# Kernel tuning notes

Hardware: AMD Instinct MI355X
Metric: run time of the kernel (lower is better)

The kernel has to match this reference:

```python
import jax, jax.numpy as jnp
import numpy as np

L, B, N, IN, H, ATTN, RED, OUT = 3, 8, 512, 64, 128, 32, 32, 3


def setup_inputs() -> dict:
    key = jax.random.key(0)
    ks = jax.random.split(key, 34)
    def rn(i, shape, s=0.05):
        return jax.random.normal(ks[i], shape, dtype=jnp.float32) * s
    inp = {
        "X": rn(0, (B, N, IN), 1.0),
        # sparse binary adjacency (avg degree ~10) and denser clique graph
        "A": (jax.random.uniform(ks[1], (B, N, N)) < 0.02).astype(jnp.float32),
        "Ac": (jax.random.uniform(ks[2], (B, N, N)) < 0.05).astype(jnp.float32),
        # topo embedding
        "embed_w": rn(3, (H, IN)), "embed_b": jnp.zeros((H,), jnp.float32),
        "topo_eps": jnp.zeros((1,), jnp.float32),
        "topo_w": rn(4, (H, H)), "topo_b": jnp.zeros((H,), jnp.float32),
        "theta": rn(5, (H, 2)),
        # per-layer dual GIN (index 0: A, index 1: Ac)
        "gin_eps": jnp.zeros((L, 2, 1), jnp.float32),
        "gin_w": rn(6, (L, 2, H, H)), "gin_b": jnp.zeros((L, 2, H), jnp.float32),
        # per-layer flexible attention
        "wo": rn(7, (L, ATTN, H)), "w1": rn(8, (L, ATTN, H)),
        "wphi": rn(9, (L, ATTN)),
        "wy_w": rn(10, (L, H, H)), "wy_b": jnp.zeros((L, H), jnp.float32),
        "we_w": rn(11, (L, H, ATTN)), "we_b": jnp.zeros((L, H), jnp.float32),
        # per-layer SE block
        "lin1_w": rn(12, (L, RED, H)), "lin1_b": jnp.zeros((L, RED), jnp.float32),
        "lin2_w": rn(13, (L, H, RED)), "lin2_b": jnp.zeros((L, H), jnp.float32),
        "mlp_w": rn(14, (L, H, H)), "mlp_b": jnp.zeros((L, H), jnp.float32),
        # node head
        "head1_w": rn(15, (H // 2, H)), "head1_b": jnp.zeros((H // 2,), jnp.float32),
        "head2_w": rn(16, (OUT, H // 2)), "head2_b": jnp.zeros((OUT,), jnp.float32),
    }
    return inp


def _lin(x, w, b=None):
    y = x @ w.T
    return y if b is None else y + b


def _gin(x, a, eps, w, b):
    # (1+eps)*X + A@X, then Linear, then ReLU
    return jax.nn.relu(_lin((1.0 + eps) * x + a @ x, w, b))


def _forward(X, A, Ac, embed_w, embed_b, topo_eps, topo_w, topo_b, theta,
             gin_eps, gin_w, gin_b, wo, w1, wphi, wy_w, wy_b, we_w, we_b,
             lin1_w, lin1_b, lin2_w, lin2_b, mlp_w, mlp_b,
             head1_w, head1_b, head2_w, head2_b):
    # TopoPositionalEmbedding (shared GIN on both graphs)
    Xh = _lin(X, embed_w, embed_b)                      # (B,N,H)
    hA = _gin(Xh, A, topo_eps[0], topo_w, topo_b)
    hAC = _gin(Xh, Ac, topo_eps[0], topo_w, topo_b)
    Xp = Xh + jnp.tanh(hA * theta[:, 0]) + jnp.tanh(hAC * theta[:, 1])

    for l in range(L):
        # dual GIN
        XA = _gin(Xp, A, gin_eps[l, 0, 0], gin_w[l, 0], gin_b[l, 0])
        XAC = _gin(Xp, Ac, gin_eps[l, 1, 0], gin_w[l, 1], gin_b[l, 1])
        # GRIT-style flexible attention
        ho = Xp @ wo[l].T                               # (B,N,ATTN)
        h1 = Xp @ w1[l].T
        e = jnp.tanh(ho[:, :, None, :] + h1[:, None, :, :])   # (B,N,N,ATTN)
        alpha = jax.nn.softmax(e @ wphi[l], axis=-1)    # (B,N,N)
        Xy = _lin(Xp, wy_w[l], wy_b[l])                 # (B,N,H)
        # sum_j alpha_ij * We(e_ij) == We(sum_j alpha_ij * e_ij) since We is affine
        # and sum_j alpha_ij == 1 (avoids the (B,N,N,H) intermediate)
        ctx = jnp.einsum('bij,bijd->bid', alpha, e)     # (B,N,ATTN)
        Xatt = alpha @ Xy + _lin(ctx, we_w[l], we_b[l])
        Xbar = XA + XAC + Xatt
        # SE gating
        y1 = jax.nn.relu(_lin(Xbar.sum(axis=1), lin1_w[l], lin1_b[l]))
        y2 = jax.nn.sigmoid(_lin(y1, lin2_w[l], lin2_b[l]))
        Xp = _lin(Xbar * y2[:, None, :], mlp_w[l], mlp_b[l])

    h = jax.nn.relu(_lin(Xp, head1_w, head1_b))
    return _lin(h, head2_w, head2_b)                    # (B,N,OUT)


def reference(X, A, Ac, embed_w, embed_b, topo_eps, topo_w, topo_b, theta,
              gin_eps, gin_w, gin_b, wo, w1, wphi, wy_w, wy_b, we_w, we_b,
              lin1_w, lin1_b, lin2_w, lin2_b, mlp_w, mlp_b,
              head1_w, head1_b, head2_w, head2_b):
    return _forward(X, A, Ac, embed_w, embed_b, topo_eps, topo_w, topo_b, theta,
                    gin_eps, gin_w, gin_b, wo, w1, wphi, wy_w, wy_b, we_w, we_b,
                    lin1_w, lin1_b, lin2_w, lin2_b, mlp_w, mlp_b,
                    head1_w, head1_b, head2_w, head2_b)
```

## Files before the change

kernel.cpp:

```cpp
#include <hip/hip_runtime.h>

#define Bc 8
#define Nc 512
#define INc 64
#define Hc 128
#define Atc 32
#define REDc 32
#define OUTc 3
#define Lc 3
#define MNc (Bc * Nc)

__device__ __forceinline__ float tanh_fast(float x) {
    float e = __expf(2.f * x);
    return 1.f - 2.f * __builtin_amdgcn_rcpf(e + 1.f);
}

template <int TM, int K, int ACT>
__global__ __launch_bounds__(256) void gemm256(
        const float* __restrict__ X, const float* __restrict__ W,
        const float* __restrict__ bias, float* __restrict__ Y,
        const float* __restrict__ scale) {
    constexpr int RPG = TM / 2;
    __shared__ float xs[TM * K];
    int m0 = blockIdx.x * TM;
    int t = threadIdx.x;
    const float* sc = scale ? scale + (size_t)(m0 >> 9) * K : nullptr;
    for (int idx4 = t; idx4 < TM * K / 4; idx4 += 256) {
        float4 v = ((const float4*)(X + (size_t)m0 * K))[idx4];
        if (sc) {
            int base = idx4 * 4;
            v.x *= sc[base & (K - 1)]; v.y *= sc[(base + 1) & (K - 1)];
            v.z *= sc[(base + 2) & (K - 1)]; v.w *= sc[(base + 3) & (K - 1)];
        }
        ((float4*)xs)[idx4] = v;
    }
    __syncthreads();
    int n = t & 127;
    int grp = t >> 7;
    float bv = bias ? bias[n] : 0.f;
    float acc[RPG];
#pragma unroll
    for (int r = 0; r < RPG; ++r) acc[r] = bv;
    const float* w = W + (size_t)n * K;
    for (int k = 0; k < K; k += 4) {
        float4 wv = *(const float4*)(w + k);
#pragma unroll
        for (int r = 0; r < RPG; ++r) {
            float4 xv = *(const float4*)(xs + (grp * RPG + r) * K + k);
            acc[r] = fmaf(xv.x, wv.x, acc[r]); acc[r] = fmaf(xv.y, wv.y, acc[r]);
            acc[r] = fmaf(xv.z, wv.z, acc[r]); acc[r] = fmaf(xv.w, wv.w, acc[r]);
        }
    }
#pragma unroll
    for (int r = 0; r < RPG; ++r) {
        float v = acc[r];
        if (ACT) v = fmaxf(v, 0.f);
        Y[(size_t)(m0 + grp * RPG + r) * 128 + n] = v;
    }
}

__global__ __launch_bounds__(128) void spmm2(
        const float* __restrict__ A, const float* __restrict__ Acg,
        const float* __restrict__ X, const float* __restrict__ eA,
        const float* __restrict__ eC, float* __restrict__ T1, float* __restrict__ T2) {
    int bi = blockIdx.x;
    int b = bi >> 9;
    int h = threadIdx.x;
    __shared__ int idxA[Nc], idxC[Nc];
    __shared__ int cntA, cntC;
    if (h == 0) { cntA = 0; cntC = 0; }
    __syncthreads();
    {
        float4 a4 = ((const float4*)(A + (size_t)bi * Nc))[h];
        if (a4.x != 0.f) idxA[atomicAdd(&cntA, 1)] = 4 * h;
        if (a4.y != 0.f) idxA[atomicAdd(&cntA, 1)] = 4 * h + 1;
        if (a4.z != 0.f) idxA[atomicAdd(&cntA, 1)] = 4 * h + 2;
        if (a4.w != 0.f) idxA[atomicAdd(&cntA, 1)] = 4 * h + 3;
        float4 c4 = ((const float4*)(Acg + (size_t)bi * Nc))[h];
        if (c4.x != 0.f) idxC[atomicAdd(&cntC, 1)] = 4 * h;
        if (c4.y != 0.f) idxC[atomicAdd(&cntC, 1)] = 4 * h + 1;
        if (c4.z != 0.f) idxC[atomicAdd(&cntC, 1)] = 4 * h + 2;
        if (c4.w != 0.f) idxC[atomicAdd(&cntC, 1)] = 4 * h + 3;
    }
    __syncthreads();
    int nA = cntA, nC = cntC;
    const float* Xb = X + (size_t)b * Nc * Hc;
    float a1 = 0.f, a2 = 0.f;
    for (int q = 0; q < nA; ++q) a1 += Xb[(size_t)idxA[q] * Hc + h];
    for (int q = 0; q < nC; ++q) a2 += Xb[(size_t)idxC[q] * Hc + h];
    size_t o = (size_t)bi * Hc + h;
    float xv = X[o];
    T1[o] = (1.f + eA[0]) * xv + a1;
    T2[o] = (1.f + eC[0]) * xv + a2;
}

__global__ __launch_bounds__(256) void gemm2_topo(
        const float* __restrict__ T1, const float* __restrict__ T2,
        const float* __restrict__ W, const float* __restrict__ bias,
        const float* __restrict__ Xh, const float* __restrict__ theta,
        float* __restrict__ Xp) {
    __shared__ float xs1[8 * Hc], xs2[8 * Hc];
    int m0 = blockIdx.x * 8;
    int t = threadIdx.x;
    for (int idx4 = t; idx4 < 8 * Hc / 4; idx4 += 256) {
        ((float4*)xs1)[idx4] = ((const float4*)(T1 + (size_t)m0 * Hc))[idx4];
        ((float4*)xs2)[idx4] = ((const float4*)(T2 + (size_t)m0 * Hc))[idx4];
    }
    __syncthreads();
    int n = t & 127, grp = t >> 7;
    float bv = bias[n];
    float ac1[4], ac2[4];
#pragma unroll
    for (int r = 0; r < 4; ++r) { ac1[r] = bv; ac2[r] = bv; }
    const float* w = W + (size_t)n * Hc;
    for (int k = 0; k < Hc; k += 4) {
        float4 wv = *(const float4*)(w + k);
#pragma unroll
        for (int r = 0; r < 4; ++r) {
            float4 x1 = *(const float4*)(xs1 + (grp * 4 + r) * Hc + k);
            float4 x2 = *(const float4*)(xs2 + (grp * 4 + r) * Hc + k);
            ac1[r] = fmaf(x1.x, wv.x, ac1[r]); ac1[r] = fmaf(x1.y, wv.y, ac1[r]);
            ac1[r] = fmaf(x1.z, wv.z, ac1[r]); ac1[r] = fmaf(x1.w, wv.w, ac1[r]);
            ac2[r] = fmaf(x2.x, wv.x, ac2[r]); ac2[r] = fmaf(x2.y, wv.y, ac2[r]);
            ac2[r] = fmaf(x2.z, wv.z, ac2[r]); ac2[r] = fmaf(x2.w, wv.w, ac2[r]);
        }
    }
    float th0 = theta[2 * n], th1 = theta[2 * n + 1];
#pragma unroll
    for (int r = 0; r < 4; ++r) {
        size_t o = (size_t)(m0 + grp * 4 + r) * Hc + n;
        float g1 = fmaxf(ac1[r], 0.f), g2 = fmaxf(ac2[r], 0.f);
        Xp[o] = Xh[o] + tanh_fast(g1 * th0) + tanh_fast(g2 * th1);
    }
}

__global__ __launch_bounds__(256) void gemm2_gin(
        const float* __restrict__ T1, const float* __restrict__ T2,
        const float* __restrict__ W1, const float* __restrict__ b1,
        const float* __restrict__ W2, const float* __restrict__ b2,
        float* __restrict__ GS) {
    __shared__ float xs1[8 * Hc], xs2[8 * Hc];
    int m0 = blockIdx.x * 8;
    int t = threadIdx.x;
    for (int idx4 = t; idx4 < 8 * Hc / 4; idx4 += 256) {
        ((float4*)xs1)[idx4] = ((const float4*)(T1 + (size_t)m0 * Hc))[idx4];
        ((float4*)xs2)[idx4] = ((const float4*)(T2 + (size_t)m0 * Hc))[idx4];
    }
    __syncthreads();
    int n = t & 127, grp = t >> 7;
    float ac1[4], ac2[4];
    float bv1 = b1[n], bv2 = b2[n];
#pragma unroll
    for (int r = 0; r < 4; ++r) { ac1[r] = bv1; ac2[r] = bv2; }
    const float* w1 = W1 + (size_t)n * Hc;
    const float* w2 = W2 + (size_t)n * Hc;
    for (int k = 0; k < Hc; k += 4) {
        float4 wv1 = *(const float4*)(w1 + k);
        float4 wv2 = *(const float4*)(w2 + k);
#pragma unroll
        for (int r = 0; r < 4; ++r) {
            float4 x1 = *(const float4*)(xs1 + (grp * 4 + r) * Hc + k);
            float4 x2 = *(const float4*)(xs2 + (grp * 4 + r) * Hc + k);
            ac1[r] = fmaf(x1.x, wv1.x, ac1[r]); ac1[r] = fmaf(x1.y, wv1.y, ac1[r]);
            ac1[r] = fmaf(x1.z, wv1.z, ac1[r]); ac1[r] = fmaf(x1.w, wv1.w, ac1[r]);
            ac2[r] = fmaf(x2.x, wv2.x, ac2[r]); ac2[r] = fmaf(x2.y, wv2.y, ac2[r]);
            ac2[r] = fmaf(x2.z, wv2.z, ac2[r]); ac2[r] = fmaf(x2.w, wv2.w, ac2[r]);
        }
    }
#pragma unroll
    for (int r = 0; r < 4; ++r) {
        size_t o = (size_t)(m0 + grp * 4 + r) * Hc + n;
        GS[o] = fmaxf(ac1[r], 0.f) + fmaxf(ac2[r], 0.f);
    }
}

__global__ __launch_bounds__(256) void qkv_gemm(
        const float* __restrict__ Xp, const float* __restrict__ wy_w,
        const float* __restrict__ wy_b, const float* __restrict__ wo,
        const float* __restrict__ w1, float* __restrict__ Xy,
        float* __restrict__ hov, float* __restrict__ h1v) {
    __shared__ float xs[8 * Hc];
    int m0 = blockIdx.x * 8;
    int t = threadIdx.x;
    for (int idx4 = t; idx4 < 8 * Hc / 4; idx4 += 256)
        ((float4*)xs)[idx4] = ((const float4*)(Xp + (size_t)m0 * Hc))[idx4];
    __syncthreads();
    {
        int n = t & 127, grp = t >> 7;
        float bv = wy_b[n];
        float acc[4];
#pragma unroll
        for (int r = 0; r < 4; ++r) acc[r] = bv;
        const float* w = wy_w + (size_t)n * Hc;
        for (int k = 0; k < Hc; k += 4) {
            float4 wv = *(const float4*)(w + k);
#pragma unroll
            for (int r = 0; r < 4; ++r) {
                float4 xv = *(const float4*)(xs + (grp * 4 + r) * Hc + k);
                acc[r] = fmaf(xv.x, wv.x, acc[r]); acc[r] = fmaf(xv.y, wv.y, acc[r]);
                acc[r] = fmaf(xv.z, wv.z, acc[r]); acc[r] = fmaf(xv.w, wv.w, acc[r]);
            }
        }
#pragma unroll
        for (int r = 0; r < 4; ++r)
            Xy[(size_t)(m0 + grp * 4 + r) * Hc + n] = acc[r];
    }
    {
        int n2 = t & 63, g2 = t >> 6;
        const float* w = (n2 < 32) ? (wo + (size_t)n2 * Hc) : (w1 + (size_t)(n2 - 32) * Hc);
        float acc[2] = {0.f, 0.f};
        for (int k = 0; k < Hc; k += 4) {
            float4 wv = *(const float4*)(w + k);
#pragma unroll
            for (int r = 0; r < 2; ++r) {
                float4 xv = *(const float4*)(xs + (g2 * 2 + r) * Hc + k);
                acc[r] = fmaf(xv.x, wv.x, acc[r]); acc[r] = fmaf(xv.y, wv.y, acc[r]);
                acc[r] = fmaf(xv.z, wv.z, acc[r]); acc[r] = fmaf(xv.w, wv.w, acc[r]);
            }
        }
#pragma unroll
        for (int r = 0; r < 2; ++r) {
            int m = m0 + g2 * 2 + r;
            float v = tanh_fast(acc[r]);
            if (n2 < 32) hov[(size_t)m * Atc + n2] = v;
            else h1v[(size_t)m * Atc + (n2 - 32)] = v;
        }
    }
}

__global__ __launch_bounds__(256) void attn_part(
        const float* __restrict__ ta, const float* __restrict__ tb,
        const float* __restrict__ wphi, const float* __restrict__ Xy,
        float* __restrict__ Pp, float* __restrict__ ctxp, float* __restrict__ wsp) {
    int blk = blockIdx.x;
    int b = blk >> 7;
    int r6 = (blk >> 1) & 63;
    int js = blk & 1;
    int i0 = r6 * 8;
    int t = threadIdx.x;
    __shared__ float als[8 * 256];
    __shared__ float4 red4[1024];
    __shared__ float tas[8 * 32];
    tas[t] = ta[((size_t)b * Nc + i0) * 32 + t];
    __syncthreads();
    {
        int i = t >> 5;
        int kq = t & 3;
        int jl = (t >> 2) & 7;
        float4 wp0 = ((const float4*)wphi)[kq * 2];
        float4 wp1 = ((const float4*)wphi)[kq * 2 + 1];
        float4 ta0 = *(const float4*)(tas + i * 32 + kq * 8);
        float4 ta1 = *(const float4*)(tas + i * 32 + kq * 8 + 4);
        const float* tbb = tb + ((size_t)b * Nc + js * 256) * 32;
        const float4* p = (const float4*)(tbb + (size_t)jl * 32 + kq * 8);
        float4 ra = p[0], rb = p[1];
        float ca[8];
#pragma unroll
        for (int q = 0; q < 8; ++q) ca[q] = 0.f;
        float wsum = 0.f;
#pragma unroll 2
        for (int jj = 0; jj < 32; ++jj) {
            float4 ha = ra, hb = rb;
            p += 64;
            if (jj < 31) { ra = p[0]; rb = p[1]; }
            float e0 = (ta0.x + ha.x) * __builtin_amdgcn_rcpf(fmaf(ta0.x, ha.x, 1.f));
            float e1 = (ta0.y + ha.y) * __builtin_amdgcn_rcpf(fmaf(ta0.y, ha.y, 1.f));
            float e2 = (ta0.z + ha.z) * __builtin_amdgcn_rcpf(fmaf(ta0.z, ha.z, 1.f));
            float e3 = (ta0.w + ha.w) * __builtin_amdgcn_rcpf(fmaf(ta0.w, ha.w, 1.f));
            float e4 = (ta1.x + hb.x) * __builtin_amdgcn_rcpf(fmaf(ta1.x, hb.x, 1.f));
            float e5 = (ta1.y + hb.y) * __builtin_amdgcn_rcpf(fmaf(ta1.y, hb.y, 1.f));
            float e6 = (ta1.z + hb.z) * __builtin_amdgcn_rcpf(fmaf(ta1.z, hb.z, 1.f));
            float e7 = (ta1.w + hb.w) * __builtin_amdgcn_rcpf(fmaf(ta1.w, hb.w, 1.f));
            float sc = e0 * wp0.x;
            sc = fmaf(e1, wp0.y, sc);
            sc = fmaf(e2, wp0.z, sc);
            sc = fmaf(e3, wp0.w, sc);
            sc = fmaf(e4, wp1.x, sc);
            sc = fmaf(e5, wp1.y, sc);
            sc = fmaf(e6, wp1.z, sc);
            sc = fmaf(e7, wp1.w, sc);
            sc += __shfl_xor(sc, 1);
            sc += __shfl_xor(sc, 2);
            float w = __expf(sc);
            if (kq == 0) als[i * 256 + jj * 8 + jl] = w;
            wsum += w;
            ca[0] = fmaf(w, e0, ca[0]);
            ca[1] = fmaf(w, e1, ca[1]);
            ca[2] = fmaf(w, e2, ca[2]);
            ca[3] = fmaf(w, e3, ca[3]);
            ca[4] = fmaf(w, e4, ca[4]);
            ca[5] = fmaf(w, e5, ca[5]);
            ca[6] = fmaf(w, e6, ca[6]);
            ca[7] = fmaf(w, e7, ca[7]);
        }
#pragma unroll
        for (int o = 16; o > 0; o >>= 1) wsum += __shfl_xor(wsum, o);
        if ((t & 31) == 0) wsp[(size_t)js * MNc + (size_t)b * Nc + i0 + i] = wsum;
#pragma unroll
        for (int q = 0; q < 8; ++q) {
            ca[q] += __shfl_xor(ca[q], 4);
            ca[q] += __shfl_xor(ca[q], 8);
            ca[q] += __shfl_xor(ca[q], 16);
        }
        if (jl == 0) {
            float* cp = ctxp + ((size_t)js * MNc + (size_t)b * Nc + i0 + i) * 32 + kq * 8;
#pragma unroll
            for (int q = 0; q < 8; ++q) cp[q] = ca[q];
        }
    }
    __syncthreads();
    {
        int h4 = t & 31, jg = t >> 5;
        const float* Xyb = Xy + ((size_t)b * Nc + js * 256) * Hc;
        float* Pb = Pp + (size_t)js * MNc * Hc;
#pragma unroll 1
        for (int c = 0; c < 2; ++c) {
            float4 acc[4];
#pragma unroll
            for (int r = 0; r < 4; ++r) acc[r] = make_float4(0.f, 0.f, 0.f, 0.f);
#pragma unroll 2
            for (int jq = 0; jq < 32; ++jq) {
                int j = jg * 32 + jq;
                float4 x = *(const float4*)(Xyb + (size_t)j * Hc + h4 * 4);
#pragma unroll
                for (int r = 0; r < 4; ++r) {
                    float av = als[(c * 4 + r) * 256 + j];
                    acc[r].x = fmaf(av, x.x, acc[r].x);
                    acc[r].y = fmaf(av, x.y, acc[r].y);
                    acc[r].z = fmaf(av, x.z, acc[r].z);
                    acc[r].w = fmaf(av, x.w, acc[r].w);
                }
            }
#pragma unroll
            for (int r = 0; r < 4; ++r) red4[jg * 128 + r * 32 + h4] = acc[r];
            __syncthreads();
            if (t < 128) {
                int ii = t >> 5, hq = t & 31;
                float4 s = red4[ii * 32 + hq];
#pragma unroll
                for (int gq = 1; gq < 8; ++gq) {
                    float4 p = red4[gq * 128 + ii * 32 + hq];
                    s.x += p.x; s.y += p.y; s.z += p.z; s.w += p.w;
                }
                *(float4*)(Pb + ((size_t)b * Nc + i0 + c * 4 + ii) * Hc + hq * 4) = s;
            }
            __syncthreads();
        }
    }
}

__global__ __launch_bounds__(256) void attn_combine(
        const float* __restrict__ Pp, const float* __restrict__ ctxp,
        const float* __restrict__ wsp, const float* __restrict__ we_w,
        const float* __restrict__ we_b, const float* __restrict__ GS,
        float* __restrict__ Xbar) {
    int m0 = blockIdx.x * 8;
    int t = threadIdx.x;
    __shared__ float ctxs[8 * 32];
    __shared__ float sinv[8];
    if (t < 8) sinv[t] = 4.f / (wsp[m0 + t] + wsp[MNc + m0 + t]);
    ctxs[t] = ctxp[(size_t)m0 * 32 + t] + ctxp[(size_t)MNc * 32 + (size_t)m0 * 32 + t];
    __syncthreads();
    int ii = t >> 5, hq = t & 31;
    size_t o = (size_t)(m0 + ii) * Hc + hq * 4;
    float4 p0 = *(const float4*)(Pp + o);
    float4 p1 = *(const float4*)(Pp + (size_t)MNc * Hc + o);
    float si = sinv[ii];
    const float* c = ctxs + ii * 32;
    float wec[4];
#pragma unroll
    for (int ho_ = 0; ho_ < 4; ++ho_) {
        const float4* wrow = (const float4*)(we_w + (size_t)(hq * 4 + ho_) * 32);
        float sv = 0.f;
#pragma unroll
        for (int q = 0; q < 8; ++q) {
            float4 w4 = wrow[q];
            sv = fmaf(w4.x, c[4 * q], sv); sv = fmaf(w4.y, c[4 * q + 1], sv);
            sv = fmaf(w4.z, c[4 * q + 2], sv); sv = fmaf(w4.w, c[4 * q + 3], sv);
        }
        wec[ho_] = sv;
    }
    float4 wb = *(const float4*)(we_b + hq * 4);
    float4 gv = *(const float4*)(GS + o);
    float4 outv;
    outv.x = (p0.x + p1.x + wec[0]) * si + wb.x + gv.x;
    outv.y = (p0.y + p1.y + wec[1]) * si + wb.y + gv.y;
    outv.z = (p0.z + p1.z + wec[2]) * si + wb.z + gv.z;
    outv.w = (p0.w + p1.w + wec[3]) * si + wb.w + gv.w;
    *(float4*)(Xbar + o) = outv;
}

__global__ __launch_bounds__(256) void se_part(
        const float* __restrict__ Xbar, float* __restrict__ part) {
    int blk = blockIdx.x;
    int b = blk >> 4, p = blk & 15;
    int t = threadIdx.x;
    int h = t & 127, half = t >> 7;
    __shared__ float s2[256];
    const float* Xb = Xbar + ((size_t)b * Nc + p * 32 + half * 16) * Hc;
    float acc = 0.f;
    for (int i = 0; i < 16; ++i) acc += Xb[(size_t)i * Hc + h];
    s2[t] = acc;
    __syncthreads();
    if (t < 128) part[(size_t)blk * Hc + t] = s2[t] + s2[t + 128];
}

__global__ __launch_bounds__(128) void se_mlp(
        const float* __restrict__ part, const float* __restrict__ l1w,
        const float* __restrict__ l1b, const float* __restrict__ l2w,
        const float* __restrict__ l2b, float* __restrict__ y2) {
    int b = blockIdx.x;
    int t = threadIdx.x;
    __shared__ float s[Hc];
    __shared__ float y1s[REDc];
    const float* pb = part + (size_t)b * 16 * Hc;
    float acc = 0.f;
#pragma unroll
    for (int p = 0; p < 16; ++p) acc += pb[p * Hc + t];
    s[t] = acc;
    __syncthreads();
    if (t < REDc) {
        float a = l1b[t];
        const float* w = l1w + (size_t)t * Hc;
        for (int k = 0; k < Hc; ++k) a = fmaf(s[k], w[k], a);
        y1s[t] = fmaxf(a, 0.f);
    }
    __syncthreads();
    {
        float a = l2b[t];
        const float* w2 = l2w + (size_t)t * REDc;
#pragma unroll
        for (int k = 0; k < REDc; ++k) a = fmaf(y1s[k], w2[k], a);
        y2[(size_t)b * Hc + t] = 1.f / (1.f + __expf(-a));
    }
}

__global__ __launch_bounds__(64) void head_kernel(const float* __restrict__ Xp, const float* __restrict__ h1w,
                            const float* __restrict__ h1b, const float* __restrict__ h2w,
                            const float* __restrict__ h2b, float* __restrict__ out) {
    int m = blockIdx.x;
    int t = threadIdx.x;
    __shared__ float xs[Hc];
    __shared__ float hs[64];
    xs[t] = Xp[(size_t)m * Hc + t];
    xs[t + 64] = Xp[(size_t)m * Hc + t + 64];
    __syncthreads();
    float a = h1b[t];
    const float* w = h1w + (size_t)t * Hc;
    for (int k = 0; k < Hc; ++k) a = fmaf(xs[k], w[k], a);
    hs[t] = fmaxf(a, 0.f);
    __syncthreads();
    if (t < OUTc) {
        float o = h2b[t];
        const float* w2 = h2w + (size_t)t * 64;
#pragma unroll
        for (int k = 0; k < 64; ++k) o = fmaf(hs[k], w2[k], o);
        out[(size_t)m * OUTc + t] = o;
    }
}

extern "C" void kernel_launch(void* const* d_in, const int* in_sizes, int n_in,
                              void* d_out, int out_size, void* d_ws, size_t ws_size,
                              hipStream_t stream) {
    const float* X       = (const float*)d_in[0];
    const float* A       = (const float*)d_in[1];
    const float* Acg     = (const float*)d_in[2];
    const float* embed_w = (const float*)d_in[3];
    const float* embed_b = (const float*)d_in[4];
    const float* topo_eps= (const float*)d_in[5];
    const float* topo_w  = (const float*)d_in[6];
    const float* topo_b  = (const float*)d_in[7];
    const float* theta   = (const float*)d_in[8];
    const float* gin_eps = (const float*)d_in[9];
    const float* gin_w   = (const float*)d_in[10];
    const float* gin_b   = (const float*)d_in[11];
    const float* wo      = (const float*)d_in[12];
    const float* w1      = (const float*)d_in[13];
    const float* wphi    = (const float*)d_in[14];
    const float* wy_w    = (const float*)d_in[15];
    const float* wy_b    = (const float*)d_in[16];
    const float* we_w    = (const float*)d_in[17];
    const float* we_b    = (const float*)d_in[18];
    const float* lin1_w  = (const float*)d_in[19];
    const float* lin1_b  = (const float*)d_in[20];
    const float* lin2_w  = (const float*)d_in[21];
    const float* lin2_b  = (const float*)d_in[22];
    const float* mlp_w   = (const float*)d_in[23];
    const float* mlp_b   = (const float*)d_in[24];
    const float* head1_w = (const float*)d_in[25];
    const float* head1_b = (const float*)d_in[26];
    const float* head2_w = (const float*)d_in[27];
    const float* head2_b = (const float*)d_in[28];
    float* out = (float*)d_out;

    float* ws = (float*)d_ws;
    const int MN = Bc * Nc;
    const size_t SZ = (size_t)MN * Hc;
    float* Xh   = ws;
    float* Xp   = Xh + SZ;
    float* T1   = Xp + SZ;
    float* T2   = T1 + SZ;
    float* GS   = T2 + SZ;
    float* Xy   = GS + SZ;
    float* hov  = Xy + SZ;
    float* h1v  = hov + (size_t)MN * Atc;
    float* y2   = h1v + (size_t)MN * Atc;
    float* part = y2 + (size_t)Bc * Hc;
    float* Pp   = part + (size_t)Bc * 16 * Hc;
    float* ctxp = Pp + 2 * SZ;
    float* wsp  = ctxp + (size_t)2 * MN * Atc;
    float* Xbar = T1;

    gemm256<8, INc, 0><<<MN / 8, 256, 0, stream>>>(X, embed_w, embed_b, Xh, nullptr);
    spmm2<<<MN, 128, 0, stream>>>(A, Acg, Xh, topo_eps, topo_eps, T1, T2);
    gemm2_topo<<<MN / 8, 256, 0, stream>>>(T1, T2, topo_w, topo_b, Xh, theta, Xp);

    for (int l = 0; l < Lc; ++l) {
        spmm2<<<MN, 128, 0, stream>>>(A, Acg, Xp, gin_eps + l * 2, gin_eps + l * 2 + 1, T1, T2);
        gemm2_gin<<<MN / 8, 256, 0, stream>>>(T1, T2,
            gin_w + (size_t)(l * 2 + 0) * Hc * Hc, gin_b + (size_t)(l * 2 + 0) * Hc,
            gin_w + (size_t)(l * 2 + 1) * Hc * Hc, gin_b + (size_t)(l * 2 + 1) * Hc, GS);
        qkv_gemm<<<MN / 8, 256, 0, stream>>>(Xp, wy_w + (size_t)l * Hc * Hc, wy_b + (size_t)l * Hc,
            wo + (size_t)l * Atc * Hc, w1 + (size_t)l * Atc * Hc, Xy, hov, h1v);
        attn_part<<<MN / 8 * 2, 256, 0, stream>>>(hov, h1v, wphi + (size_t)l * Atc, Xy,
                                                  Pp, ctxp, wsp);
        attn_combine<<<MN / 8, 256, 0, stream>>>(Pp, ctxp, wsp,
                                                 we_w + (size_t)l * Hc * Atc,
                                                 we_b + (size_t)l * Hc, GS, Xbar);
        se_part<<<Bc * 16, 256, 0, stream>>>(Xbar, part);
        se_mlp<<<Bc, 128, 0, stream>>>(part, lin1_w + (size_t)l * REDc * Hc, lin1_b + (size_t)l * REDc,
                                       lin2_w + (size_t)l * Hc * REDc, lin2_b + (size_t)l * Hc, y2);
        gemm256<8, Hc, 0><<<MN / 8, 256, 0, stream>>>(Xbar, mlp_w + (size_t)l * Hc * Hc,
                                                      mlp_b + (size_t)l * Hc, Xp, y2);
    }
    head_kernel<<<MN, 64, 0, stream>>>(Xp, head1_w, head1_b, head2_w, head2_b, out);
}
```

Before: 452.2 us.

## Fuse layer GEMMs, split attention into four key chunks, fold SE partial sums into combine

Merges the GIN and QKV projection GEMMs into a single kernel, and merges the attention combine with the SE partial column sums. This removes two launches per layer and one re-read of Xbar. Attention is split into four key-range chunks instead of two, doubling the block count for more parallelism. In exchange it writes and reads twice as many partial buffers, and the SE MLP must sum 64 partials instead of 16.

```diff
diff --git a/kernel.cpp b/kernel.cpp
--- a/kernel.cpp
+++ b/kernel.cpp
@@ -134,59 +134,51 @@
     }
 }
 
-__global__ __launch_bounds__(256) void gemm2_gin(
+__global__ __launch_bounds__(256) void layer_gemms(
         const float* __restrict__ T1, const float* __restrict__ T2,
         const float* __restrict__ W1, const float* __restrict__ b1,
         const float* __restrict__ W2, const float* __restrict__ b2,
-        float* __restrict__ GS) {
-    __shared__ float xs1[8 * Hc], xs2[8 * Hc];
+        const float* __restrict__ Xp, const float* __restrict__ wy_w,
+        const float* __restrict__ wy_b, const float* __restrict__ wo,
+        const float* __restrict__ w1a, float* __restrict__ GS,
+        float* __restrict__ Xy, float* __restrict__ hov, float* __restrict__ h1v) {
+    __shared__ float xs1[8 * Hc], xs2[8 * Hc], xs[8 * Hc];
     int m0 = blockIdx.x * 8;
     int t = threadIdx.x;
     for (int idx4 = t; idx4 < 8 * Hc / 4; idx4 += 256) {
         ((float4*)xs1)[idx4] = ((const float4*)(T1 + (size_t)m0 * Hc))[idx4];
         ((float4*)xs2)[idx4] = ((const float4*)(T2 + (size_t)m0 * Hc))[idx4];
+        ((float4*)xs)[idx4]  = ((const float4*)(Xp + (size_t)m0 * Hc))[idx4];
     }
     __syncthreads();
     int n = t & 127, grp = t >> 7;
-    float ac1[4], ac2[4];
-    float bv1 = b1[n], bv2 = b2[n];
-#pragma unroll
-    for (int r = 0; r < 4; ++r) { ac1[r] = bv1; ac2[r] = bv2; }
-    const float* w1 = W1 + (size_t)n * Hc;
-    const float* w2 = W2 + (size_t)n * Hc;
-    for (int k = 0; k < Hc; k += 4) {
-        float4 wv1 = *(const float4*)(w1 + k);
-        float4 wv2 = *(const float4*)(w2 + k);
+    {
+        float ac1[4], ac2[4];
+        float bv1 = b1[n], bv2 = b2[n];
+#pragma unroll
+        for (int r = 0; r < 4; ++r) { ac1[r] = bv1; ac2[r] = bv2; }
+        const float* w1 = W1 + (size_t)n * Hc;
+        const float* w2 = W2 + (size_t)n * Hc;
+        for (int k = 0; k < Hc; k += 4) {
+            float4 wv1 = *(const float4*)(w1 + k);
+            float4 wv2 = *(const float4*)(w2 + k);
+#pragma unroll
+            for (int r = 0; r < 4; ++r) {
+                float4 x1 = *(const float4*)(xs1 + (grp * 4 + r) * Hc + k);
+                float4 x2 = *(const float4*)(xs2 + (grp * 4 + r) * Hc + k);
+                ac1[r] = fmaf(x1.x, wv1.x, ac1[r]); ac1[r] = fmaf(x1.y, wv1.y, ac1[r]);
+                ac1[r] = fmaf(x1.z, wv1.z, ac1[r]); ac1[r] = fmaf(x1.w, wv1.w, ac1[r]);
+                ac2[r] = fmaf(x2.x, wv2.x, ac2[r]); ac2[r] = fmaf(x2.y, wv2.y, ac2[r]);
+                ac2[r] = fmaf(x2.z, wv2.z, ac2[r]); ac2[r] = fmaf(x2.w, wv2.w, ac2[r]);
+            }
+        }
 #pragma unroll
         for (int r = 0; r < 4; ++r) {
-            float4 x1 = *(const float4*)(xs1 + (grp * 4 + r) * Hc + k);
-            float4 x2 = *(const float4*)(xs2 + (grp * 4 + r) * Hc + k);
-            ac1[r] = fmaf(x1.x, wv1.x, ac1[r]); ac1[r] = fmaf(x1.y, wv1.y, ac1[r]);
-            ac1[r] = fmaf(x1.z, wv1.z, ac1[r]); ac1[r] = fmaf(x1.w, wv1.w, ac1[r]);
-            ac2[r] = fmaf(x2.x, wv2.x, ac2[r]); ac2[r] = fmaf(x2.y, wv2.y, ac2[r]);
-            ac2[r] = fmaf(x2.z, wv2.z, ac2[r]); ac2[r] = fmaf(x2.w, wv2.w, ac2[r]);
-        }
-    }
-#pragma unroll
-    for (int r = 0; r < 4; ++r) {
-        size_t o = (size_t)(m0 + grp * 4 + r) * Hc + n;
-        GS[o] = fmaxf(ac1[r], 0.f) + fmaxf(ac2[r], 0.f);
-    }
-}
-
-__global__ __launch_bounds__(256) void qkv_gemm(
-        const float* __restrict__ Xp, const float* __restrict__ wy_w,
-        const float* __restrict__ wy_b, const float* __restrict__ wo,
-        const float* __restrict__ w1, float* __restrict__ Xy,
-        float* __restrict__ hov, float* __restrict__ h1v) {
-    __shared__ float xs[8 * Hc];
-    int m0 = blockIdx.x * 8;
-    int t = threadIdx.x;
-    for (int idx4 = t; idx4 < 8 * Hc / 4; idx4 += 256)
-        ((float4*)xs)[idx4] = ((const float4*)(Xp + (size_t)m0 * Hc))[idx4];
-    __syncthreads();
-    {
-        int n = t & 127, grp = t >> 7;
+            size_t o = (size_t)(m0 + grp * 4 + r) * Hc + n;
+            GS[o] = fmaxf(ac1[r], 0.f) + fmaxf(ac2[r], 0.f);
+        }
+    }
+    {
         float bv = wy_b[n];
         float acc[4];
 #pragma unroll
@@ -207,7 +199,7 @@
     }
     {
         int n2 = t & 63, g2 = t >> 6;
-        const float* w = (n2 < 32) ? (wo + (size_t)n2 * Hc) : (w1 + (size_t)(n2 - 32) * Hc);
+        const float* w = (n2 < 32) ? (wo + (size_t)n2 * Hc) : (w1a + (size_t)(n2 - 32) * Hc);
         float acc[2] = {0.f, 0.f};
         for (int k = 0; k < Hc; k += 4) {
             float4 wv = *(const float4*)(w + k);
@@ -233,12 +225,12 @@
         const float* __restrict__ wphi, const float* __restrict__ Xy,
         float* __restrict__ Pp, float* __restrict__ ctxp, float* __restrict__ wsp) {
     int blk = blockIdx.x;
-    int b = blk >> 7;
-    int r6 = (blk >> 1) & 63;
-    int js = blk & 1;
+    int b = blk >> 8;
+    int r6 = (blk >> 2) & 63;
+    int js = blk & 3;
     int i0 = r6 * 8;
     int t = threadIdx.x;
-    __shared__ float als[8 * 256];
+    __shared__ float als[8 * 128];
     __shared__ float4 red4[1024];
     __shared__ float tas[8 * 32];
     tas[t] = ta[((size_t)b * Nc + i0) * 32 + t];
@@ -251,7 +243,7 @@
         float4 wp1 = ((const float4*)wphi)[kq * 2 + 1];
         float4 ta0 = *(const float4*)(tas + i * 32 + kq * 8);
         float4 ta1 = *(const float4*)(tas + i * 32 + kq * 8 + 4);
-        const float* tbb = tb + ((size_t)b * Nc + js * 256) * 32;
+        const float* tbb = tb + ((size_t)b * Nc + js * 128) * 32;
         const float4* p = (const float4*)(tbb + (size_t)jl * 32 + kq * 8);
         float4 ra = p[0], rb = p[1];
         float ca[8];
@@ -259,10 +251,10 @@
         for (int q = 0; q < 8; ++q) ca[q] = 0.f;
         float wsum = 0.f;
 #pragma unroll 2
-        for (int jj = 0; jj < 32; ++jj) {
+        for (int jj = 0; jj < 16; ++jj) {
             float4 ha = ra, hb = rb;
             p += 64;
-            if (jj < 31) { ra = p[0]; rb = p[1]; }
+            if (jj < 15) { ra = p[0]; rb = p[1]; }
             float e0 = (ta0.x + ha.x) * __builtin_amdgcn_rcpf(fmaf(ta0.x, ha.x, 1.f));
             float e1 = (ta0.y + ha.y) * __builtin_amdgcn_rcpf(fmaf(ta0.y, ha.y, 1.f));
             float e2 = (ta0.z + ha.z) * __builtin_amdgcn_rcpf(fmaf(ta0.z, ha.z, 1.f));
@@ -282,7 +274,7 @@
             sc += __shfl_xor(sc, 1);
             sc += __shfl_xor(sc, 2);
             float w = __expf(sc);
-            if (kq == 0) als[i * 256 + jj * 8 + jl] = w;
+            if (kq == 0) als[i * 128 + jj * 8 + jl] = w;
             wsum += w;
             ca[0] = fmaf(w, e0, ca[0]);
             ca[1] = fmaf(w, e1, ca[1]);
@@ -311,7 +303,7 @@
     __syncthreads();
     {
         int h4 = t & 31, jg = t >> 5;
-        const float* Xyb = Xy + ((size_t)b * Nc + js * 256) * Hc;
+        const float* Xyb = Xy + ((size_t)b * Nc + js * 128) * Hc;
         float* Pb = Pp + (size_t)js * MNc * Hc;
 #pragma unroll 1
         for (int c = 0; c < 2; ++c) {
@@ -319,12 +311,12 @@
 #pragma unroll
             for (int r = 0; r < 4; ++r) acc[r] = make_float4(0.f, 0.f, 0.f, 0.f);
 #pragma unroll 2
-            for (int jq = 0; jq < 32; ++jq) {
-                int j = jg * 32 + jq;
+            for (int jq = 0; jq < 16; ++jq) {
+                int j = jg * 16 + jq;
                 float4 x = *(const float4*)(Xyb + (size_t)j * Hc + h4 * 4);
 #pragma unroll
                 for (int r = 0; r < 4; ++r) {
-                    float av = als[(c * 4 + r) * 256 + j];
+                    float av = als[(c * 4 + r) * 128 + j];
                     acc[r].x = fmaf(av, x.x, acc[r].x);
                     acc[r].y = fmaf(av, x.y, acc[r].y);
                     acc[r].z = fmaf(av, x.z, acc[r].z);
@@ -349,22 +341,38 @@
     }
 }
 
-__global__ __launch_bounds__(256) void attn_combine(
+__global__ __launch_bounds__(256) void combine_se(
         const float* __restrict__ Pp, const float* __restrict__ ctxp,
         const float* __restrict__ wsp, const float* __restrict__ we_w,
         const float* __restrict__ we_b, const float* __restrict__ GS,
-        float* __restrict__ Xbar) {
-    int m0 = blockIdx.x * 8;
+        float* __restrict__ Xbar, float* __restrict__ part) {
+    int blk = blockIdx.x;
+    int m0 = blk * 8;
     int t = threadIdx.x;
     __shared__ float ctxs[8 * 32];
     __shared__ float sinv[8];
-    if (t < 8) sinv[t] = 4.f / (wsp[m0 + t] + wsp[MNc + m0 + t]);
-    ctxs[t] = ctxp[(size_t)m0 * 32 + t] + ctxp[(size_t)MNc * 32 + (size_t)m0 * 32 + t];
+    __shared__ float4 sred[256];
+    if (t < 8) {
+        float ws = 0.f;
+#pragma unroll
+        for (int s = 0; s < 4; ++s) ws += wsp[(size_t)s * MNc + m0 + t];
+        sinv[t] = 4.f / ws;
+    }
+    {
+        float c = 0.f;
+#pragma unroll
+        for (int s = 0; s < 4; ++s) c += ctxp[((size_t)s * MNc + m0) * 32 + t];
+        ctxs[t] = c;
+    }
     __syncthreads();
     int ii = t >> 5, hq = t & 31;
     size_t o = (size_t)(m0 + ii) * Hc + hq * 4;
-    float4 p0 = *(const float4*)(Pp + o);
-    float4 p1 = *(const float4*)(Pp + (size_t)MNc * Hc + o);
+    float4 ps = *(const float4*)(Pp + o);
+#pragma unroll
+    for (int s = 1; s < 4; ++s) {
+        float4 p = *(const float4*)(Pp + (size_t)s * MNc * Hc + o);
+        ps.x += p.x; ps.y += p.y; ps.z += p.z; ps.w += p.w;
+    }
     float si = sinv[ii];
     const float* c = ctxs + ii * 32;
     float wec[4];
@@ -383,26 +391,22 @@
     float4 wb = *(const float4*)(we_b + hq * 4);
     float4 gv = *(const float4*)(GS + o);
     float4 outv;
-    outv.x = (p0.x + p1.x + wec[0]) * si + wb.x + gv.x;
-    outv.y = (p0.y + p1.y + wec[1]) * si + wb.y + gv.y;
-    outv.z = (p0.z + p1.z + wec[2]) * si + wb.z + gv.z;
-    outv.w = (p0.w + p1.w + wec[3]) * si + wb.w + gv.w;
+    outv.x = (ps.x + wec[0]) * si + wb.x + gv.x;
+    outv.y = (ps.y + wec[1]) * si + wb.y + gv.y;
+    outv.z = (ps.z + wec[2]) * si + wb.z + gv.z;
+    outv.w = (ps.w + wec[3]) * si + wb.w + gv.w;
     *(float4*)(Xbar + o) = outv;
-}
-
-__global__ __launch_bounds__(256) void se_part(
-        const float* __restrict__ Xbar, float* __restrict__ part) {
-    int blk = blockIdx.x;
-    int b = blk >> 4, p = blk & 15;
-    int t = threadIdx.x;
-    int h = t & 127, half = t >> 7;
-    __shared__ float s2[256];
-    const float* Xb = Xbar + ((size_t)b * Nc + p * 32 + half * 16) * Hc;
-    float acc = 0.f;
-    for (int i = 0; i < 16; ++i) acc += Xb[(size_t)i * Hc + h];
-    s2[t] = acc;
-    __syncthreads();
-    if (t < 128) part[(size_t)blk * Hc + t] = s2[t] + s2[t + 128];
+    sred[ii * 32 + hq] = outv;
+    __syncthreads();
+    if (t < 32) {
+        float4 s0 = sred[t];
+#pragma unroll
+        for (int g = 1; g < 8; ++g) {
+            float4 p = sred[g * 32 + t];
+            s0.x += p.x; s0.y += p.y; s0.z += p.z; s0.w += p.w;
+        }
+        *(float4*)(part + (size_t)blk * Hc + t * 4) = s0;
+    }
 }
 
 __global__ __launch_bounds__(128) void se_mlp(
@@ -413,10 +417,9 @@
     int t = threadIdx.x;
     __shared__ float s[Hc];
     __shared__ float y1s[REDc];
-    const float* pb = part + (size_t)b * 16 * Hc;
+    const float* pb = part + (size_t)b * 64 * Hc;
     float acc = 0.f;
-#pragma unroll
-    for (int p = 0; p < 16; ++p) acc += pb[p * Hc + t];
+    for (int p = 0; p < 64; ++p) acc += pb[p * Hc + t];
     s[t] = acc;
     __syncthreads();
     if (t < REDc) {
@@ -506,9 +509,9 @@
     float* h1v  = hov + (size_t)MN * Atc;
     float* y2   = h1v + (size_t)MN * Atc;
     float* part = y2 + (size_t)Bc * Hc;
-    float* Pp   = part + (size_t)Bc * 16 * Hc;
-    float* ctxp = Pp + 2 * SZ;
-    float* wsp  = ctxp + (size_t)2 * MN * Atc;
+    float* Pp   = part + (size_t)Bc * 64 * Hc;
+    float* ctxp = Pp + 4 * SZ;
+    float* wsp  = ctxp + (size_t)4 * MN * Atc;
     float* Xbar = T1;
 
     gemm256<8, INc, 0><<<MN / 8, 256, 0, stream>>>(X, embed_w, embed_b, Xh, nullptr);
@@ -517,17 +520,17 @@
 
     for (int l = 0; l < Lc; ++l) {
         spmm2<<<MN, 128, 0, stream>>>(A, Acg, Xp, gin_eps + l * 2, gin_eps + l * 2 + 1, T1, T2);
-        gemm2_gin<<<MN / 8, 256, 0, stream>>>(T1, T2,
+        layer_gemms<<<MN / 8, 256, 0, stream>>>(T1, T2,
             gin_w + (size_t)(l * 2 + 0) * Hc * Hc, gin_b + (size_t)(l * 2 + 0) * Hc,
-            gin_w + (size_t)(l * 2 + 1) * Hc * Hc, gin_b + (size_t)(l * 2 + 1) * Hc, GS);
-        qkv_gemm<<<MN / 8, 256, 0, stream>>>(Xp, wy_w + (size_t)l * Hc * Hc, wy_b + (size_t)l * Hc,
-            wo + (size_t)l * Atc * Hc, w1 + (size_t)l * Atc * Hc, Xy, hov, h1v);
-        attn_part<<<MN / 8 * 2, 256, 0, stream>>>(hov, h1v, wphi + (size_t)l * Atc, Xy,
+            gin_w + (size_t)(l * 2 + 1) * Hc * Hc, gin_b + (size_t)(l * 2 + 1) * Hc,
+            Xp, wy_w + (size_t)l * Hc * Hc, wy_b + (size_t)l * Hc,
+            wo + (size_t)l * Atc * Hc, w1 + (size_t)l * Atc * Hc,
+            GS, Xy, hov, h1v);
+        attn_part<<<MN / 8 * 4, 256, 0, stream>>>(hov, h1v, wphi + (size_t)l * Atc, Xy,
                                                   Pp, ctxp, wsp);
-        attn_combine<<<MN / 8, 256, 0, stream>>>(Pp, ctxp, wsp,
-                                                 we_w + (size_t)l * Hc * Atc,
-                                                 we_b + (size_t)l * Hc, GS, Xbar);
-        se_part<<<Bc * 16, 256, 0, stream>>>(Xbar, part);
+        combine_se<<<MN / 8, 256, 0, stream>>>(Pp, ctxp, wsp,
+                                               we_w + (size_t)l * Hc * Atc,
+                                               we_b + (size_t)l * Hc, GS, Xbar, part);
         se_mlp<<<Bc, 128, 0, stream>>>(part, lin1_w + (size_t)l * REDc * Hc, lin1_b + (size_t)l * REDc,
                                        lin2_w + (size_t)l * Hc * REDc, lin2_b + (size_t)l * Hc, y2);
         gemm256<8, Hc, 0><<<MN / 8, 256, 0, stream>>>(Xbar, mlp_w + (size_t)l * Hc * Hc,
```

Measured after the change: 445.9 us. Within noise of the previous version (-1.4%).
